# Kernel tuning notes

Hardware: AMD Instinct MI355X
Metric: run time of the kernel (lower is better)

The kernel has to match this reference:

```python
import jax, jax.numpy as jnp
import numpy as np

B, C, H, W = 8, 256, 128, 128
HEADS, DIM_HEAD = 4, 32
HID = HEADS * DIM_HEAD  # 128


def setup_inputs() -> dict:
    key = jax.random.key(0)
    k1, k2, k3, k4 = jax.random.split(key, 4)
    x = jax.random.normal(k1, (B, C, H, W), dtype=jnp.float32)
    # 1x1 conv weights stored as [out_ch, in_ch]
    w_qkv = jax.random.normal(k2, (3 * HID, C), dtype=jnp.float32) * (1.0 / np.sqrt(C))
    w_out = jax.random.normal(k3, (C, HID), dtype=jnp.float32) * (1.0 / np.sqrt(HID))
    b_out = jax.random.normal(k4, (C,), dtype=jnp.float32) * 0.01
    return {"x": x, "w_qkv": w_qkv, "w_out": w_out, "b_out": b_out}


def reference(x, w_qkv, w_out, b_out):
    b, c, h, w = x.shape
    n = h * w
    # 1x1 conv == channel matmul
    qkv = jnp.einsum('oc,bchw->bohw', w_qkv, x)  # [b, 3*HID, h, w]
    q, k, v = jnp.split(qkv, 3, axis=1)
    # rearrange 'b (heads d) h w -> b heads d (h w)'
    def to_heads(t):
        return t.reshape(b, HEADS, DIM_HEAD, n)
    q, k, v = to_heads(q), to_heads(k), to_heads(v)
    k = jax.nn.softmax(k, axis=-1)  # over spatial n
    # q_scale is False: q used as-is
    context = jnp.einsum('bhdn,bhen->bhde', k, v)   # [b, heads, d, e] small
    out = jnp.einsum('bhde,bhdn->bhen', context, q)  # [b, heads, e, n]
    out = out.reshape(b, HID, h, w)
    out = jnp.einsum('oc,bchw->bohw', w_out, out) + b_out[None, :, None, None]
    return out
```

## Files before the change

kernel.cpp:

```cpp
#include <hip/hip_runtime.h>
#include <stdint.h>

#define BB 8
#define CIN 256
#define NSP 16384
#define HID 128

typedef __bf16 bfrag __attribute__((ext_vector_type(8)));
typedef float  f32x4 __attribute__((ext_vector_type(4)));

__device__ __forceinline__ unsigned short f2bf(float f) {
  union { float f; unsigned int u; } v; v.f = f;
  unsigned int u = v.u;
  return (unsigned short)((u + 0x7FFFu + ((u >> 16) & 1u)) >> 16);
}

__global__ __launch_bounds__(512, 2) void la_fused(const float* __restrict__ x,
                                                   const float* __restrict__ w_qkv,
                                                   unsigned short* __restrict__ qT,
                                                   float* __restrict__ ctxp,
                                                   float* __restrict__ sums) {
  __shared__ __align__(16) union {
    struct { unsigned short Wt[384][40]; unsigned short Xb[128][40]; } g;
    struct { unsigned short Lk[64][136]; unsigned short Lv[64][136];
             float Pc[4][1024]; } e;
  } sh;
  const int chunk = blockIdx.x;
  const int n0 = chunk * 128;
  const int b = blockIdx.y;
  const int t = threadIdx.x;
  const int lane = t & 63, wv = t >> 6;
  const int l15 = lane & 15, q = lane >> 4;
  const int cl = t & 31;
  const int n16 = (t >> 5) * 8;
  const float* xp = x + (size_t)b * CIN * NSP + n0;
  f32x4 acc[3][8];
#pragma unroll
  for (int i = 0; i < 3; ++i)
#pragma unroll
    for (int j = 0; j < 8; ++j) acc[i][j] = 0.0f;

  for (int kc = 0; kc < 8; ++kc) {
#pragma unroll
    for (int i = 0; i < 3; ++i) {
      const int id = t + i * 512;
      const int row = id >> 2, c8 = (id & 3) * 8;
      const float* wr = w_qkv + (size_t)row * CIN + kc * 32 + c8;
      const float4 wa = *(const float4*)wr;
      const float4 wb4 = *(const float4*)(wr + 4);
      ushort4 p0, p1;
      p0.x = f2bf(wa.x); p0.y = f2bf(wa.y); p0.z = f2bf(wa.z); p0.w = f2bf(wa.w);
      p1.x = f2bf(wb4.x); p1.y = f2bf(wb4.y); p1.z = f2bf(wb4.z); p1.w = f2bf(wb4.w);
      *(ushort4*)&sh.g.Wt[row][c8] = p0;
      *(ushort4*)&sh.g.Wt[row][c8 + 4] = p1;
    }
    const float* xr = xp + (size_t)(kc * 32 + cl) * NSP + n16;
    const float4 xa = *(const float4*)xr;
    const float4 xb4 = *(const float4*)(xr + 4);
    sh.g.Xb[n16 + 0][cl] = f2bf(xa.x);
    sh.g.Xb[n16 + 1][cl] = f2bf(xa.y);
    sh.g.Xb[n16 + 2][cl] = f2bf(xa.z);
    sh.g.Xb[n16 + 3][cl] = f2bf(xa.w);
    sh.g.Xb[n16 + 4][cl] = f2bf(xb4.x);
    sh.g.Xb[n16 + 5][cl] = f2bf(xb4.y);
    sh.g.Xb[n16 + 6][cl] = f2bf(xb4.z);
    sh.g.Xb[n16 + 7][cl] = f2bf(xb4.w);
    __syncthreads();
    bfrag a0 = *(const bfrag*)&sh.g.Wt[wv * 16 + l15][q * 8];
    bfrag a1 = *(const bfrag*)&sh.g.Wt[128 + wv * 16 + l15][q * 8];
    bfrag a2 = *(const bfrag*)&sh.g.Wt[256 + wv * 16 + l15][q * 8];
    bfrag bb[8];
#pragma unroll
    for (int ni = 0; ni < 8; ++ni) bb[ni] = *(const bfrag*)&sh.g.Xb[ni * 16 + l15][q * 8];
#pragma unroll
    for (int ni = 0; ni < 8; ++ni) {
      acc[0][ni] = __builtin_amdgcn_mfma_f32_16x16x32_bf16(a0, bb[ni], acc[0][ni], 0, 0, 0);
      acc[1][ni] = __builtin_amdgcn_mfma_f32_16x16x32_bf16(a1, bb[ni], acc[1][ni], 0, 0, 0);
      acc[2][ni] = __builtin_amdgcn_mfma_f32_16x16x32_bf16(a2, bb[ni], acc[2][ni], 0, 0, 0);
    }
    __syncthreads();
  }

  {
    unsigned short* qb = qT + (size_t)b * NSP * HID;
    const int qrow = wv * 16 + q * 4;
#pragma unroll
    for (int ni = 0; ni < 8; ++ni) {
      const int n = n0 + ni * 16 + l15;
      ushort4 pk;
      pk.x = f2bf(acc[0][ni][0]);
      pk.y = f2bf(acc[0][ni][1]);
      pk.z = f2bf(acc[0][ni][2]);
      pk.w = f2bf(acc[0][ni][3]);
      *(ushort4*)(qb + (size_t)n * HID + qrow) = pk;
    }
  }
  {
    float sp[4] = {0.f, 0.f, 0.f, 0.f};
#pragma unroll
    for (int ni = 0; ni < 8; ++ni)
#pragma unroll
      for (int rg = 0; rg < 4; ++rg) sp[rg] += __expf(acc[1][ni][rg]);
#pragma unroll
    for (int rg = 0; rg < 4; ++rg) {
      float s = sp[rg];
      s += __shfl_down(s, 8, 16);
      s += __shfl_down(s, 4, 16);
      s += __shfl_down(s, 2, 16);
      s += __shfl_down(s, 1, 16);
      if (l15 == 0) atomicAdd(&sums[b * 128 + wv * 16 + q * 4 + rg], s);
    }
  }
  float* cp = ctxp + ((size_t)chunk * 32 + b * 4) * 1024;
#pragma unroll
  for (int ph = 0; ph < 2; ++ph) {
    if ((wv >> 2) == ph) {
      const int r = (wv & 3) * 16 + q * 4;
#pragma unroll
      for (int ni = 0; ni < 8; ++ni)
#pragma unroll
        for (int rg = 0; rg < 4; ++rg) {
          sh.e.Lk[r + rg][ni * 16 + l15] = f2bf(__expf(acc[1][ni][rg]));
          sh.e.Lv[r + rg][ni * 16 + l15] = f2bf(acc[2][ni][rg]);
        }
    }
    __syncthreads();
    const int hl = wv >> 2, nq = wv & 3;
    f32x4 c2[2][2];
    c2[0][0] = 0.f; c2[0][1] = 0.f; c2[1][0] = 0.f; c2[1][1] = 0.f;
    bfrag ka[2], vb[2];
#pragma unroll
    for (int d2 = 0; d2 < 2; ++d2)
      ka[d2] = *(const bfrag*)&sh.e.Lk[hl * 32 + d2 * 16 + l15][nq * 32 + q * 8];
#pragma unroll
    for (int e2 = 0; e2 < 2; ++e2)
      vb[e2] = *(const bfrag*)&sh.e.Lv[hl * 32 + e2 * 16 + l15][nq * 32 + q * 8];
#pragma unroll
    for (int d2 = 0; d2 < 2; ++d2)
#pragma unroll
      for (int e2 = 0; e2 < 2; ++e2)
        c2[d2][e2] = __builtin_amdgcn_mfma_f32_16x16x32_bf16(ka[d2], vb[e2], c2[d2][e2], 0, 0, 0);
    const int slot = hl * 2 + (nq & 1);
    if (nq < 2) {
#pragma unroll
      for (int d2 = 0; d2 < 2; ++d2)
#pragma unroll
        for (int e2 = 0; e2 < 2; ++e2)
#pragma unroll
          for (int rg = 0; rg < 4; ++rg)
            sh.e.Pc[slot][(d2 * 16 + q * 4 + rg) * 32 + e2 * 16 + l15] = c2[d2][e2][rg];
    }
    __syncthreads();
    if (nq >= 2) {
#pragma unroll
      for (int d2 = 0; d2 < 2; ++d2)
#pragma unroll
        for (int e2 = 0; e2 < 2; ++e2)
#pragma unroll
          for (int rg = 0; rg < 4; ++rg)
            sh.e.Pc[slot][(d2 * 16 + q * 4 + rg) * 32 + e2 * 16 + l15] += c2[d2][e2][rg];
    }
    __syncthreads();
    for (int idx = t; idx < 2048; idx += 512) {
      const int h2 = idx >> 10, pos = idx & 1023;
      cp[(ph * 2 + h2) * 1024 + pos] = sh.e.Pc[h2 * 2][pos] + sh.e.Pc[h2 * 2 + 1][pos];
    }
    __syncthreads();
  }
}

__global__ __launch_bounds__(256) void la_reduce(const float* __restrict__ ctxp,
                                                 float* __restrict__ ctxu) {
  const int gid = blockIdx.x * 256 + threadIdx.x;
  float s = 0.f;
#pragma unroll 8
  for (int c = 0; c < 128; ++c) s += ctxp[(size_t)c * 32768 + gid];
  ctxu[gid] = s;
}

__global__ __launch_bounds__(128) void la_weff(const float* __restrict__ w_out,
                                               const float* __restrict__ ctxu,
                                               const float* __restrict__ sums,
                                               unsigned short* __restrict__ weff) {
  const int o = blockIdx.x;
  const int b = blockIdx.y;
  const int cp = threadIdx.x;
  const int h = cp >> 5, d = cp & 31;
  const float* wrow = w_out + (size_t)o * HID + h * 32;
  const float* crow = ctxu + ((size_t)(b * 4 + h) * 32 + d) * 32;
  float s = 0.f;
#pragma unroll 8
  for (int e = 0; e < 32; ++e) s += wrow[e] * crow[e];
  s *= (1.0f / sums[b * 128 + h * 32 + d]);
  weff[((size_t)b * 256 + o) * HID + cp] = f2bf(s);
}

__global__ __launch_bounds__(256) void la_out_gemm(const unsigned short* __restrict__ weff,
                                                   const unsigned short* __restrict__ qT,
                                                   const float* __restrict__ b_out,
                                                   float* __restrict__ out) {
  __shared__ __align__(16) unsigned short At[128][40];
  __shared__ __align__(16) unsigned short Bt[128][40];
  const int mblk = blockIdx.x;
  const int n0 = blockIdx.y * 128;
  const int b = blockIdx.z;
  const int t = threadIdx.x;
  const int lane = t & 63, wv = t >> 6;
  const int wm = (wv >> 1) * 64, wn = (wv & 1) * 64;
  const int l15 = lane & 15, q = lane >> 4;
  f32x4 acc[4][4];
#pragma unroll
  for (int i = 0; i < 4; ++i)
#pragma unroll
    for (int j = 0; j < 4; ++j) acc[i][j] = 0.0f;
  const unsigned short* abase = weff + ((size_t)b * 256 + mblk * 128) * HID;
  const unsigned short* bbase = qT + ((size_t)b * NSP + n0) * HID;
  const int r = t >> 1, hh = (t & 1) * 16;
  for (int kc = 0; kc < 4; ++kc) {
    const int ko = kc * 32 + hh;
    uint4 a0 = *(const uint4*)(abase + (size_t)r * HID + ko);
    uint4 a1 = *(const uint4*)(abase + (size_t)r * HID + ko + 8);
    uint4 b0 = *(const uint4*)(bbase + (size_t)r * HID + ko);
    uint4 b1 = *(const uint4*)(bbase + (size_t)r * HID + ko + 8);
    *(uint4*)&At[r][hh] = a0;
    *(uint4*)&At[r][hh + 8] = a1;
    *(uint4*)&Bt[r][hh] = b0;
    *(uint4*)&Bt[r][hh + 8] = b1;
    __syncthreads();
    bfrag a[4], bf[4];
#pragma unroll
    for (int mi = 0; mi < 4; ++mi) a[mi] = *(const bfrag*)&At[wm + mi * 16 + l15][q * 8];
#pragma unroll
    for (int ni = 0; ni < 4; ++ni) bf[ni] = *(const bfrag*)&Bt[wn + ni * 16 + l15][q * 8];
#pragma unroll
    for (int mi = 0; mi < 4; ++mi)
#pragma unroll
      for (int ni = 0; ni < 4; ++ni)
        acc[mi][ni] = __builtin_amdgcn_mfma_f32_16x16x32_bf16(a[mi], bf[ni], acc[mi][ni], 0, 0, 0);
    __syncthreads();
  }
  float* obase = out + ((size_t)b * 256 + mblk * 128) * NSP;
#pragma unroll
  for (int mi = 0; mi < 4; ++mi) {
    const int ob = wm + mi * 16 + q * 4;
    const float4 bias = *(const float4*)(b_out + mblk * 128 + ob);
    float ba[4] = {bias.x, bias.y, bias.z, bias.w};
#pragma unroll
    for (int ni = 0; ni < 4; ++ni) {
      const int n = n0 + wn + ni * 16 + l15;
#pragma unroll
      for (int rg = 0; rg < 4; ++rg)
        obase[(size_t)(ob + rg) * NSP + n] = acc[mi][ni][rg] + ba[rg];
    }
  }
}


extern "C" void kernel_launch(void* const* d_in, const int* in_sizes, int n_in,
                              void* d_out, int out_size, void* d_ws, size_t ws_size,
                              hipStream_t stream) {
  (void)in_sizes; (void)n_in; (void)out_size; (void)ws_size;
  const float* x     = (const float*)d_in[0];
  const float* w_qkv = (const float*)d_in[1];
  const float* w_out = (const float*)d_in[2];
  const float* b_out = (const float*)d_in[3];
  float* out = (float*)d_out;
  char* ws = (char*)d_ws;
  unsigned short* qT   = (unsigned short*)(ws);
  float* ctxp          = (float*)(ws + 33554432);
  float* ctxu          = (float*)(ws + 50331648);
  float* sums          = (float*)(ws + 50462720);
  unsigned short* weff = (unsigned short*)(ws + 50466816);

  hipMemsetAsync(sums, 0, 4096, stream);
  la_fused<<<dim3(NSP / 128, BB), dim3(512), 0, stream>>>(x, w_qkv, qT, ctxp, sums);
  la_reduce<<<dim3(128), dim3(256), 0, stream>>>(ctxp, ctxu);
  la_weff<<<dim3(256, BB), dim3(128), 0, stream>>>(w_out, ctxu, sums, weff);
  la_out_gemm<<<dim3(2, NSP / 128, BB), dim3(256), 0, stream>>>(weff, qT, b_out, out);
}
```

Measured before the change: 346.1 us.

## Fold Q projection into combined output weight and recompute from x

The Q projection is removed from the first pass: it now computes only K and V and no longer writes a bf16 qT buffer. A new small kernel multiplies the effective output weight by the Q rows of w_qkv, giving a per-batch 256x256 combined weight, and the final GEMM reads x directly with K=256. This drops the write and re-read of the 32 MB qT buffer in exchange for doubling the K dimension of the output GEMM and reading x twice. The change also prefetches the next x tile into registers and raises the occupancy hint to 4 blocks.

```diff
diff --git a/kernel.cpp b/kernel.cpp
--- a/kernel.cpp
+++ b/kernel.cpp
@@ -15,13 +15,12 @@
   return (unsigned short)((u + 0x7FFFu + ((u >> 16) & 1u)) >> 16);
 }
 
-__global__ __launch_bounds__(512, 2) void la_fused(const float* __restrict__ x,
+__global__ __launch_bounds__(512, 4) void la_fused(const float* __restrict__ x,
                                                    const float* __restrict__ w_qkv,
-                                                   unsigned short* __restrict__ qT,
                                                    float* __restrict__ ctxp,
                                                    float* __restrict__ sums) {
   __shared__ __align__(16) union {
-    struct { unsigned short Wt[384][40]; unsigned short Xb[128][40]; } g;
+    struct { unsigned short Wt[256][40]; unsigned short Xb[128][40]; } g;
     struct { unsigned short Lk[64][136]; unsigned short Lv[64][136];
              float Pc[4][1024]; } e;
   } sh;
@@ -34,18 +33,34 @@
   const int cl = t & 31;
   const int n16 = (t >> 5) * 8;
   const float* xp = x + (size_t)b * CIN * NSP + n0;
-  f32x4 acc[3][8];
-#pragma unroll
-  for (int i = 0; i < 3; ++i)
+  const float* wkv = w_qkv + (size_t)128 * CIN;
+  f32x4 acc[2][8];
+#pragma unroll
+  for (int i = 0; i < 2; ++i)
 #pragma unroll
     for (int j = 0; j < 8; ++j) acc[i][j] = 0.0f;
 
+  float4 xa0, xa1;
+  {
+    const float* xr = xp + (size_t)cl * NSP + n16;
+    xa0 = *(const float4*)xr;
+    xa1 = *(const float4*)(xr + 4);
+  }
+
   for (int kc = 0; kc < 8; ++kc) {
-#pragma unroll
-    for (int i = 0; i < 3; ++i) {
+    sh.g.Xb[n16 + 0][cl] = f2bf(xa0.x);
+    sh.g.Xb[n16 + 1][cl] = f2bf(xa0.y);
+    sh.g.Xb[n16 + 2][cl] = f2bf(xa0.z);
+    sh.g.Xb[n16 + 3][cl] = f2bf(xa0.w);
+    sh.g.Xb[n16 + 4][cl] = f2bf(xa1.x);
+    sh.g.Xb[n16 + 5][cl] = f2bf(xa1.y);
+    sh.g.Xb[n16 + 6][cl] = f2bf(xa1.z);
+    sh.g.Xb[n16 + 7][cl] = f2bf(xa1.w);
+#pragma unroll
+    for (int i = 0; i < 2; ++i) {
       const int id = t + i * 512;
       const int row = id >> 2, c8 = (id & 3) * 8;
-      const float* wr = w_qkv + (size_t)row * CIN + kc * 32 + c8;
+      const float* wr = wkv + (size_t)row * CIN + kc * 32 + c8;
       const float4 wa = *(const float4*)wr;
       const float4 wb4 = *(const float4*)(wr + 4);
       ushort4 p0, p1;
@@ -54,53 +69,34 @@
       *(ushort4*)&sh.g.Wt[row][c8] = p0;
       *(ushort4*)&sh.g.Wt[row][c8 + 4] = p1;
     }
-    const float* xr = xp + (size_t)(kc * 32 + cl) * NSP + n16;
-    const float4 xa = *(const float4*)xr;
-    const float4 xb4 = *(const float4*)(xr + 4);
-    sh.g.Xb[n16 + 0][cl] = f2bf(xa.x);
-    sh.g.Xb[n16 + 1][cl] = f2bf(xa.y);
-    sh.g.Xb[n16 + 2][cl] = f2bf(xa.z);
-    sh.g.Xb[n16 + 3][cl] = f2bf(xa.w);
-    sh.g.Xb[n16 + 4][cl] = f2bf(xb4.x);
-    sh.g.Xb[n16 + 5][cl] = f2bf(xb4.y);
-    sh.g.Xb[n16 + 6][cl] = f2bf(xb4.z);
-    sh.g.Xb[n16 + 7][cl] = f2bf(xb4.w);
-    __syncthreads();
+    __syncthreads();
+    if (kc < 7) {
+      const float* xr = xp + (size_t)((kc + 1) * 32 + cl) * NSP + n16;
+      xa0 = *(const float4*)xr;
+      xa1 = *(const float4*)(xr + 4);
+    }
     bfrag a0 = *(const bfrag*)&sh.g.Wt[wv * 16 + l15][q * 8];
     bfrag a1 = *(const bfrag*)&sh.g.Wt[128 + wv * 16 + l15][q * 8];
-    bfrag a2 = *(const bfrag*)&sh.g.Wt[256 + wv * 16 + l15][q * 8];
-    bfrag bb[8];
-#pragma unroll
-    for (int ni = 0; ni < 8; ++ni) bb[ni] = *(const bfrag*)&sh.g.Xb[ni * 16 + l15][q * 8];
 #pragma unroll
     for (int ni = 0; ni < 8; ++ni) {
-      acc[0][ni] = __builtin_amdgcn_mfma_f32_16x16x32_bf16(a0, bb[ni], acc[0][ni], 0, 0, 0);
-      acc[1][ni] = __builtin_amdgcn_mfma_f32_16x16x32_bf16(a1, bb[ni], acc[1][ni], 0, 0, 0);
-      acc[2][ni] = __builtin_amdgcn_mfma_f32_16x16x32_bf16(a2, bb[ni], acc[2][ni], 0, 0, 0);
-    }
-    __syncthreads();
-  }
-
-  {
-    unsigned short* qb = qT + (size_t)b * NSP * HID;
-    const int qrow = wv * 16 + q * 4;
-#pragma unroll
-    for (int ni = 0; ni < 8; ++ni) {
-      const int n = n0 + ni * 16 + l15;
-      ushort4 pk;
-      pk.x = f2bf(acc[0][ni][0]);
-      pk.y = f2bf(acc[0][ni][1]);
-      pk.z = f2bf(acc[0][ni][2]);
-      pk.w = f2bf(acc[0][ni][3]);
-      *(ushort4*)(qb + (size_t)n * HID + qrow) = pk;
-    }
-  }
+      bfrag bbv = *(const bfrag*)&sh.g.Xb[ni * 16 + l15][q * 8];
+      acc[0][ni] = __builtin_amdgcn_mfma_f32_16x16x32_bf16(a0, bbv, acc[0][ni], 0, 0, 0);
+      acc[1][ni] = __builtin_amdgcn_mfma_f32_16x16x32_bf16(a1, bbv, acc[1][ni], 0, 0, 0);
+    }
+    __syncthreads();
+  }
+
+#pragma unroll
+  for (int ni = 0; ni < 8; ++ni)
+#pragma unroll
+    for (int rg = 0; rg < 4; ++rg) acc[0][ni][rg] = __expf(acc[0][ni][rg]);
+
   {
     float sp[4] = {0.f, 0.f, 0.f, 0.f};
 #pragma unroll
     for (int ni = 0; ni < 8; ++ni)
 #pragma unroll
-      for (int rg = 0; rg < 4; ++rg) sp[rg] += __expf(acc[1][ni][rg]);
+      for (int rg = 0; rg < 4; ++rg) sp[rg] += acc[0][ni][rg];
 #pragma unroll
     for (int rg = 0; rg < 4; ++rg) {
       float s = sp[rg];
@@ -120,8 +116,8 @@
       for (int ni = 0; ni < 8; ++ni)
 #pragma unroll
         for (int rg = 0; rg < 4; ++rg) {
-          sh.e.Lk[r + rg][ni * 16 + l15] = f2bf(__expf(acc[1][ni][rg]));
-          sh.e.Lv[r + rg][ni * 16 + l15] = f2bf(acc[2][ni][rg]);
+          sh.e.Lk[r + rg][ni * 16 + l15] = f2bf(acc[0][ni][rg]);
+          sh.e.Lv[r + rg][ni * 16 + l15] = f2bf(acc[1][ni][rg]);
         }
     }
     __syncthreads();
@@ -181,7 +177,7 @@
 __global__ __launch_bounds__(128) void la_weff(const float* __restrict__ w_out,
                                                const float* __restrict__ ctxu,
                                                const float* __restrict__ sums,
-                                               unsigned short* __restrict__ weff) {
+                                               float* __restrict__ weffF) {
   const int o = blockIdx.x;
   const int b = blockIdx.y;
   const int cp = threadIdx.x;
@@ -192,58 +188,91 @@
 #pragma unroll 8
   for (int e = 0; e < 32; ++e) s += wrow[e] * crow[e];
   s *= (1.0f / sums[b * 128 + h * 32 + d]);
-  weff[((size_t)b * 256 + o) * HID + cp] = f2bf(s);
-}
-
-__global__ __launch_bounds__(256) void la_out_gemm(const unsigned short* __restrict__ weff,
-                                                   const unsigned short* __restrict__ qT,
-                                                   const float* __restrict__ b_out,
-                                                   float* __restrict__ out) {
-  __shared__ __align__(16) unsigned short At[128][40];
+  weffF[((size_t)b * 256 + o) * HID + cp] = s;
+}
+
+__global__ __launch_bounds__(256) void la_wcomb(const float* __restrict__ weffF,
+                                                const float* __restrict__ w_qkv,
+                                                unsigned short* __restrict__ wcomb) {
+  __shared__ float ws[128];
+  const int o = blockIdx.x;
+  const int b = blockIdx.y;
+  const int t = threadIdx.x;
+  if (t < 128) ws[t] = weffF[((size_t)b * 256 + o) * HID + t];
+  __syncthreads();
+  float s = 0.f;
+#pragma unroll 8
+  for (int hd = 0; hd < 128; ++hd) s += ws[hd] * w_qkv[(size_t)hd * CIN + t];
+  wcomb[((size_t)b * 256 + o) * 256 + t] = f2bf(s);
+}
+
+__global__ __launch_bounds__(512, 4) void la_out(const unsigned short* __restrict__ wcomb,
+                                                 const float* __restrict__ x,
+                                                 const float* __restrict__ b_out,
+                                                 float* __restrict__ out) {
+  __shared__ __align__(16) unsigned short At[256][40];
   __shared__ __align__(16) unsigned short Bt[128][40];
-  const int mblk = blockIdx.x;
-  const int n0 = blockIdx.y * 128;
-  const int b = blockIdx.z;
+  const int n0 = blockIdx.x * 128;
+  const int b = blockIdx.y;
   const int t = threadIdx.x;
   const int lane = t & 63, wv = t >> 6;
-  const int wm = (wv >> 1) * 64, wn = (wv & 1) * 64;
   const int l15 = lane & 15, q = lane >> 4;
+  const int wm = (wv & 3) * 64;
+  const int wn = (wv >> 2) * 64;
+  const int cl = t & 31, n16 = (t >> 5) * 8;
+  const float* xp = x + (size_t)b * CIN * NSP + n0;
+  const unsigned short* abase = wcomb + (size_t)b * 256 * 256;
   f32x4 acc[4][4];
 #pragma unroll
   for (int i = 0; i < 4; ++i)
 #pragma unroll
     for (int j = 0; j < 4; ++j) acc[i][j] = 0.0f;
-  const unsigned short* abase = weff + ((size_t)b * 256 + mblk * 128) * HID;
-  const unsigned short* bbase = qT + ((size_t)b * NSP + n0) * HID;
-  const int r = t >> 1, hh = (t & 1) * 16;
-  for (int kc = 0; kc < 4; ++kc) {
-    const int ko = kc * 32 + hh;
-    uint4 a0 = *(const uint4*)(abase + (size_t)r * HID + ko);
-    uint4 a1 = *(const uint4*)(abase + (size_t)r * HID + ko + 8);
-    uint4 b0 = *(const uint4*)(bbase + (size_t)r * HID + ko);
-    uint4 b1 = *(const uint4*)(bbase + (size_t)r * HID + ko + 8);
-    *(uint4*)&At[r][hh] = a0;
-    *(uint4*)&At[r][hh + 8] = a1;
-    *(uint4*)&Bt[r][hh] = b0;
-    *(uint4*)&Bt[r][hh + 8] = b1;
-    __syncthreads();
-    bfrag a[4], bf[4];
+
+  float4 xa0, xa1;
+  {
+    const float* xr = xp + (size_t)cl * NSP + n16;
+    xa0 = *(const float4*)xr;
+    xa1 = *(const float4*)(xr + 4);
+  }
+
+  for (int kc = 0; kc < 8; ++kc) {
+    Bt[n16 + 0][cl] = f2bf(xa0.x);
+    Bt[n16 + 1][cl] = f2bf(xa0.y);
+    Bt[n16 + 2][cl] = f2bf(xa0.z);
+    Bt[n16 + 3][cl] = f2bf(xa0.w);
+    Bt[n16 + 4][cl] = f2bf(xa1.x);
+    Bt[n16 + 5][cl] = f2bf(xa1.y);
+    Bt[n16 + 6][cl] = f2bf(xa1.z);
+    Bt[n16 + 7][cl] = f2bf(xa1.w);
+#pragma unroll
+    for (int i = 0; i < 2; ++i) {
+      const int id = t + i * 512;
+      const int row = id >> 2, c8 = (id & 3) * 8;
+      *(uint4*)&At[row][c8] = *(const uint4*)(abase + (size_t)row * 256 + kc * 32 + c8);
+    }
+    __syncthreads();
+    if (kc < 7) {
+      const float* xr = xp + (size_t)((kc + 1) * 32 + cl) * NSP + n16;
+      xa0 = *(const float4*)xr;
+      xa1 = *(const float4*)(xr + 4);
+    }
+    bfrag a[4];
 #pragma unroll
     for (int mi = 0; mi < 4; ++mi) a[mi] = *(const bfrag*)&At[wm + mi * 16 + l15][q * 8];
 #pragma unroll
-    for (int ni = 0; ni < 4; ++ni) bf[ni] = *(const bfrag*)&Bt[wn + ni * 16 + l15][q * 8];
-#pragma unroll
-    for (int mi = 0; mi < 4; ++mi)
-#pragma unroll
-      for (int ni = 0; ni < 4; ++ni)
-        acc[mi][ni] = __builtin_amdgcn_mfma_f32_16x16x32_bf16(a[mi], bf[ni], acc[mi][ni], 0, 0, 0);
-    __syncthreads();
-  }
-  float* obase = out + ((size_t)b * 256 + mblk * 128) * NSP;
+    for (int ni = 0; ni < 4; ++ni) {
+      bfrag bbv = *(const bfrag*)&Bt[wn + ni * 16 + l15][q * 8];
+#pragma unroll
+      for (int mi = 0; mi < 4; ++mi)
+        acc[mi][ni] = __builtin_amdgcn_mfma_f32_16x16x32_bf16(a[mi], bbv, acc[mi][ni], 0, 0, 0);
+    }
+    __syncthreads();
+  }
+  float* obase = out + (size_t)b * 256 * NSP;
 #pragma unroll
   for (int mi = 0; mi < 4; ++mi) {
     const int ob = wm + mi * 16 + q * 4;
-    const float4 bias = *(const float4*)(b_out + mblk * 128 + ob);
+    const float4 bias = *(const float4*)(b_out + ob);
     float ba[4] = {bias.x, bias.y, bias.z, bias.w};
 #pragma unroll
     for (int ni = 0; ni < 4; ++ni) {
@@ -266,15 +295,16 @@
   const float* b_out = (const float*)d_in[3];
   float* out = (float*)d_out;
   char* ws = (char*)d_ws;
-  unsigned short* qT   = (unsigned short*)(ws);
-  float* ctxp          = (float*)(ws + 33554432);
-  float* ctxu          = (float*)(ws + 50331648);
-  float* sums          = (float*)(ws + 50462720);
-  unsigned short* weff = (unsigned short*)(ws + 50466816);
+  float* ctxp          = (float*)(ws);
+  float* ctxu          = (float*)(ws + 16777216);
+  float* sums          = (float*)(ws + 16908288);
+  float* weffF         = (float*)(ws + 16912384);
+  unsigned short* wcomb = (unsigned short*)(ws + 17960960);
 
   hipMemsetAsync(sums, 0, 4096, stream);
-  la_fused<<<dim3(NSP / 128, BB), dim3(512), 0, stream>>>(x, w_qkv, qT, ctxp, sums);
+  la_fused<<<dim3(NSP / 128, BB), dim3(512), 0, stream>>>(x, w_qkv, ctxp, sums);
   la_reduce<<<dim3(128), dim3(256), 0, stream>>>(ctxp, ctxu);
-  la_weff<<<dim3(256, BB), dim3(128), 0, stream>>>(w_out, ctxu, sums, weff);
-  la_out_gemm<<<dim3(2, NSP / 128, BB), dim3(256), 0, stream>>>(weff, qT, b_out, out);
-}
+  la_weff<<<dim3(256, BB), dim3(128), 0, stream>>>(w_out, ctxu, sums, weffF);
+  la_wcomb<<<dim3(256, BB), dim3(256), 0, stream>>>(weffF, w_qkv, wcomb);
+  la_out<<<dim3(NSP / 128, BB), dim3(512), 0, stream>>>(wcomb, x, b_out, out);
+}
```

After: 346.6 us. About the same (+0.2%).
